# Kernel tuning notes

Measured on AMD Instinct MI355X. Metric: run time of the kernel, lower is better.

## Reference

```python
import jax, jax.numpy as jnp
import numpy as np

N_NODES = 100000
N_EDGES = 3200000
IN_FEATS = 128
OUT_FEATS = 64


def setup_inputs() -> dict:
    key = jax.random.key(0)
    k1, k2, k3, k4 = jax.random.split(key, 4)
    in_feat = jax.random.normal(k1, (N_NODES, IN_FEATS), dtype=jnp.float32)
    src = jax.random.randint(k2, (N_EDGES,), 0, N_NODES, dtype=jnp.int64)
    dst = jax.random.randint(k3, (N_EDGES,), 0, N_NODES, dtype=jnp.int64)
    W = jax.random.normal(k4, (IN_FEATS, OUT_FEATS), dtype=jnp.float32) / np.sqrt(IN_FEATS)
    b = jnp.zeros((OUT_FEATS,), dtype=jnp.float32)
    return {"in_feat": in_feat, "src": src, "dst": dst, "W": W, "b": b}


def reference(in_feat, src, dst, W, b):
    n = in_feat.shape[0]
    ones = jnp.ones_like(src, dtype=in_feat.dtype)
    # DGL GraphConv norm='both': scale by out-degree(src)^-1/2 before agg,
    # in-degree(dst)^-1/2 after agg. Clamp degree to >=1 for isolated nodes.
    deg_out = jnp.maximum(jax.ops.segment_sum(ones, src, num_segments=n), 1.0)
    deg_in = jnp.maximum(jax.ops.segment_sum(ones, dst, num_segments=n), 1.0)
    # in_feats > out_feats => apply W first (mult-first path in DGL)
    xw = in_feat @ W  # [N, out]
    msg = xw[src] * jax.lax.rsqrt(deg_out)[src][:, None]  # [E, out]
    agg = jax.ops.segment_sum(msg, dst, num_segments=n)  # [N, out]
    h = agg * jax.lax.rsqrt(deg_in)[:, None] + b
    return jax.nn.relu(h)
```

## Files before the change

### kernel.cpp

```cpp
#include <hip/hip_runtime.h>
#include <hip/hip_bf16.h>


constexpr int N_NODES = 100000;
constexpr int N_EDGES = 3200000;
constexpr int IN_F    = 128;
constexpr int OUT_F   = 64;
constexpr int BUCKET_NODES = 256;
constexpr int NB   = (N_NODES + BUCKET_NODES - 1) / BUCKET_NODES;
constexpr int CAPB = 10240;
constexpr int C_CHUNK  = 4096;
constexpr int C_BLOCKS = (N_EDGES + C_CHUNK - 1) / C_CHUNK;
constexpr int R_TILE   = 16;

__global__ __launch_bounds__(512) void partition_kernel(
        const int* __restrict__ src, const int* __restrict__ dst,
        int* __restrict__ bucket_cnt, int* __restrict__ bucket_cnt2,
        unsigned* __restrict__ pairs, unsigned char* __restrict__ sbytes) {
    __shared__ int l_cnt [NB], l_base [NB], l_pos [NB], g_base [NB];
    __shared__ int l_cnt2[NB], l_base2[NB], l_pos2[NB], g_base2[NB];
    __shared__ int wsum_s[8];
    __shared__ unsigned buf[C_CHUNK];
    __shared__ unsigned short bkt_of[C_CHUNK];
    __shared__ unsigned char  bbuf[C_CHUNK];
    __shared__ unsigned short bkt2_of[C_CHUNK];
    const int tid  = threadIdx.x;
    const int lane = tid & 63;
    const int wid  = tid >> 6;
    const long e0 = (long)blockIdx.x * C_CHUNK;
    const int  cn = (int)min((long)C_CHUNK, (long)N_EDGES - e0);

    for (int i = tid; i < NB; i += 512) { l_cnt[i] = 0; l_cnt2[i] = 0; }
    __syncthreads();

    unsigned r_pk[8];
    short    r_bk[8];
    #pragma unroll
    for (int k = 0; k < 8; ++k) {
        int i = tid + k * 512;
        r_bk[k] = -1;
        if (i < cn) {
            int d = dst[e0 + i];
            int s = src[e0 + i];
            int bk = d >> 8;
            r_bk[k] = (short)bk;
            r_pk[k] = ((unsigned)(d & 255) << 17) | (unsigned)s;
            atomicAdd(&l_cnt[bk], 1);
            atomicAdd(&l_cnt2[s >> 8], 1);
        }
    }
    __syncthreads();

    {
        int v = (tid < NB) ? l_cnt[tid] : 0;
        int inc = v;
        #pragma unroll
        for (int off = 1; off < 64; off <<= 1) {
            int t = __shfl_up(inc, off);
            if (lane >= off) inc += t;
        }
        if (lane == 63) wsum_s[wid] = inc;
        __syncthreads();
        int woff = 0;
        #pragma unroll
        for (int w = 0; w < 8; ++w) if (w < wid) woff += wsum_s[w];
        int excl = woff + inc - v;
        if (tid < NB) {
            l_base[tid] = excl;
            l_pos[tid]  = excl;
            g_base[tid] = v ? atomicAdd(&bucket_cnt[tid], v) : 0;
        }
    }
    __syncthreads();
    {
        int v = (tid < NB) ? l_cnt2[tid] : 0;
        int inc = v;
        #pragma unroll
        for (int off = 1; off < 64; off <<= 1) {
            int t = __shfl_up(inc, off);
            if (lane >= off) inc += t;
        }
        if (lane == 63) wsum_s[wid] = inc;
        __syncthreads();
        int woff = 0;
        #pragma unroll
        for (int w = 0; w < 8; ++w) if (w < wid) woff += wsum_s[w];
        int excl = woff + inc - v;
        if (tid < NB) {
            l_base2[tid] = excl;
            l_pos2[tid]  = excl;
            g_base2[tid] = v ? atomicAdd(&bucket_cnt2[tid], v) : 0;
        }
    }
    __syncthreads();

    #pragma unroll
    for (int k = 0; k < 8; ++k) {
        if (r_bk[k] >= 0) {
            unsigned pk = r_pk[k];
            int p = atomicAdd(&l_pos[(int)r_bk[k]], 1);
            buf[p] = pk;
            bkt_of[p] = (unsigned short)r_bk[k];
            int bk2 = (int)((pk >> 8) & 0x1FF);
            int p2 = atomicAdd(&l_pos2[bk2], 1);
            bbuf[p2] = (unsigned char)(pk & 255);
            bkt2_of[p2] = (unsigned short)bk2;
        }
    }
    __syncthreads();

    for (int i = tid; i < cn; i += 512) {
        int bk = bkt_of[i];
        int gp = g_base[bk] + (i - l_base[bk]);
        if (gp < CAPB)
            pairs[(long)bk * CAPB + gp] = buf[i];
        int b2 = bkt2_of[i];
        int gp2 = g_base2[b2] + (i - l_base2[b2]);
        if (gp2 < CAPB)
            sbytes[(long)b2 * CAPB + gp2] = bbuf[i];
    }
}

__global__ __launch_bounds__(256) void count_kernel(
        const unsigned char* __restrict__ sbytes, const int* __restrict__ bucket_cnt2,
        int* __restrict__ deg_out_i) {
    __shared__ int hist[BUCKET_NODES];
    const int tid = threadIdx.x;
    const int bk  = blockIdx.x;
    hist[tid] = 0;
    __syncthreads();

    const int cnt = min(bucket_cnt2[bk], CAPB);
    const unsigned* sb4 = (const unsigned*)(sbytes + (long)bk * CAPB);
    const int n4 = cnt >> 2;
    for (int i = tid; i < n4; i += 256) {
        unsigned u = sb4[i];
        atomicAdd(&hist[u & 255], 1);
        atomicAdd(&hist[(u >> 8) & 255], 1);
        atomicAdd(&hist[(u >> 16) & 255], 1);
        atomicAdd(&hist[u >> 24], 1);
    }
    for (int i = (n4 << 2) + tid; i < cnt; i += 256)
        atomicAdd(&hist[sbytes[(long)bk * CAPB + i]], 1);
    __syncthreads();

    const int node = bk * BUCKET_NODES + tid;
    if (node < N_NODES) deg_out_i[node] = hist[tid];
}

__global__ __launch_bounds__(256) void gemm_scale_kernel(
        const float* __restrict__ x, const float* __restrict__ W,
        const int* __restrict__ deg_out_i, __hip_bfloat16* __restrict__ sxw) {
    __shared__ float Wl[IN_F * OUT_F];
    __shared__ float xl[R_TILE * IN_F];
    const int tid = threadIdx.x;
    for (int i = tid; i < IN_F * OUT_F; i += 256) Wl[i] = W[i];

    const int sub = tid >> 6;
    const int col = tid & 63;
    const int n_groups = N_NODES / R_TILE;

    for (int g = blockIdx.x; g < n_groups; g += gridDim.x) {
        __syncthreads();
        const float4* xg = (const float4*)(x + (long)g * R_TILE * IN_F);
        float4* xl4 = (float4*)xl;
        xl4[tid]       = xg[tid];
        xl4[tid + 256] = xg[tid + 256];
        __syncthreads();

        float a0 = 0.0f, a1 = 0.0f, a2 = 0.0f, a3 = 0.0f;
        const float* xr = &xl[sub * 4 * IN_F];
        #pragma unroll
        for (int k4 = 0; k4 < IN_F / 4; ++k4) {
            float4 x0 = ((const float4*)xr)[k4];
            float4 x1 = ((const float4*)(xr + IN_F))[k4];
            float4 x2 = ((const float4*)(xr + 2 * IN_F))[k4];
            float4 x3 = ((const float4*)(xr + 3 * IN_F))[k4];
            float w0 = Wl[(k4 * 4 + 0) * OUT_F + col];
            float w1 = Wl[(k4 * 4 + 1) * OUT_F + col];
            float w2 = Wl[(k4 * 4 + 2) * OUT_F + col];
            float w3 = Wl[(k4 * 4 + 3) * OUT_F + col];
            a0 += x0.x * w0 + x0.y * w1 + x0.z * w2 + x0.w * w3;
            a1 += x1.x * w0 + x1.y * w1 + x1.z * w2 + x1.w * w3;
            a2 += x2.x * w0 + x2.y * w1 + x2.z * w2 + x2.w * w3;
            a3 += x3.x * w0 + x3.y * w1 + x3.z * w2 + x3.w * w3;
        }

        const int r0 = g * R_TILE + sub * 4;
        int d0 = deg_out_i[r0 + 0], d1 = deg_out_i[r0 + 1];
        int d2 = deg_out_i[r0 + 2], d3 = deg_out_i[r0 + 3];
        float s0 = rsqrtf((float)(d0 < 1 ? 1 : d0));
        float s1 = rsqrtf((float)(d1 < 1 ? 1 : d1));
        float s2 = rsqrtf((float)(d2 < 1 ? 1 : d2));
        float s3 = rsqrtf((float)(d3 < 1 ? 1 : d3));
        sxw[(long)(r0 + 0) * OUT_F + col] = __float2bfloat16(a0 * s0);
        sxw[(long)(r0 + 1) * OUT_F + col] = __float2bfloat16(a1 * s1);
        sxw[(long)(r0 + 2) * OUT_F + col] = __float2bfloat16(a2 * s2);
        sxw[(long)(r0 + 3) * OUT_F + col] = __float2bfloat16(a3 * s3);
    }
}

__global__ __launch_bounds__(512) void csr_kernel(
        unsigned* __restrict__ pairs, const int* __restrict__ bucket_cnt,
        int* __restrict__ row_beg, int* __restrict__ row_deg) {
    __shared__ int hist[BUCKET_NODES];
    __shared__ int cur[BUCKET_NODES];
    __shared__ int wsum[4];
    __shared__ unsigned buf[CAPB];
    const int tid  = threadIdx.x;
    const int lane = tid & 63;
    const int wid  = tid >> 6;
    const int bk   = blockIdx.x;
    const long base = (long)bk * CAPB;
    const int cnt  = min(bucket_cnt[bk], CAPB);

    if (tid < 256) hist[tid] = 0;
    __syncthreads();

    for (int i = tid; i < cnt; i += 512) {
        unsigned e = pairs[base + i];
        buf[i] = e;
        atomicAdd(&hist[e >> 17], 1);
    }
    __syncthreads();

    int v = (tid < 256) ? hist[tid] : 0;
    int inc = v;
    #pragma unroll
    for (int off = 1; off < 64; off <<= 1) {
        int t = __shfl_up(inc, off);
        if (lane >= off) inc += t;
    }
    if (tid < 256 && lane == 63) wsum[wid] = inc;
    __syncthreads();
    if (tid < 256) {
        int woff = 0;
        #pragma unroll
        for (int w = 0; w < 4; ++w) if (w < wid) woff += wsum[w];
        int excl = woff + inc - v;
        cur[tid] = excl;
        const int node = bk * BUCKET_NODES + tid;
        if (node < N_NODES) {
            row_beg[node] = (int)(base + excl);
            row_deg[node] = v;
        }
    }
    __syncthreads();

    for (int i = tid; i < cnt; i += 512) {
        unsigned e = buf[i];
        int p = atomicAdd(&cur[e >> 17], 1);
        pairs[base + p] = e & 0x1FFFF;
    }
}

#define ACC8(u)                                   \
    a0 += __uint_as_float((u).x << 16);           \
    a1 += __uint_as_float((u).x & 0xFFFF0000u);   \
    a2 += __uint_as_float((u).y << 16);           \
    a3 += __uint_as_float((u).y & 0xFFFF0000u);   \
    a4 += __uint_as_float((u).z << 16);           \
    a5 += __uint_as_float((u).z & 0xFFFF0000u);   \
    a6 += __uint_as_float((u).w << 16);           \
    a7 += __uint_as_float((u).w & 0xFFFF0000u);

__global__ __launch_bounds__(256) void gather_kernel(
        const int* __restrict__ row_beg, const int* __restrict__ row_deg,
        const unsigned* __restrict__ csr_src, const uint4* __restrict__ sxw4,
        const float* __restrict__ b, float* __restrict__ out) {
    const int lane = threadIdx.x & 63;
    const int node = blockIdx.x * 4 + (threadIdx.x >> 6);
    if (node >= N_NODES) return;

    const int eo = lane >> 3;
    const int c  = lane & 7;

    const int beg = row_beg[node];
    const int deg = row_deg[node];
    const int end = beg + deg;

    float a0 = 0, a1 = 0, a2 = 0, a3 = 0, a4 = 0, a5 = 0, a6 = 0, a7 = 0;

    int j = beg;
    for (; j + 16 <= end; j += 16) {
        unsigned sA = csr_src[j + eo];
        unsigned sB = csr_src[j + 8 + eo];
        uint4 uA = sxw4[(long)sA * 8 + c];
        uint4 uB = sxw4[(long)sB * 8 + c];
        ACC8(uA)
        ACC8(uB)
    }
    for (; j + 8 <= end; j += 8) {
        unsigned s = csr_src[j + eo];
        uint4 u = sxw4[(long)s * 8 + c];
        ACC8(u)
    }
    if (j < end) {
        int e = j + eo;
        if (e < end) {
            unsigned s = csr_src[e];
            uint4 u = sxw4[(long)s * 8 + c];
            ACC8(u)
        }
    }

    #pragma unroll
    for (int off = 8; off < 64; off <<= 1) {
        a0 += __shfl_xor(a0, off);
        a1 += __shfl_xor(a1, off);
        a2 += __shfl_xor(a2, off);
        a3 += __shfl_xor(a3, off);
        a4 += __shfl_xor(a4, off);
        a5 += __shfl_xor(a5, off);
        a6 += __shfl_xor(a6, off);
        a7 += __shfl_xor(a7, off);
    }

    if (lane < 8) {
        float d = (float)(deg < 1 ? 1 : deg);
        float s = rsqrtf(d);
        float4 b0 = ((const float4*)b)[c * 2];
        float4 b1 = ((const float4*)b)[c * 2 + 1];
        float4 o0, o1;
        o0.x = a0 * s + b0.x; o0.x = o0.x > 0.0f ? o0.x : 0.0f;
        o0.y = a1 * s + b0.y; o0.y = o0.y > 0.0f ? o0.y : 0.0f;
        o0.z = a2 * s + b0.z; o0.z = o0.z > 0.0f ? o0.z : 0.0f;
        o0.w = a3 * s + b0.w; o0.w = o0.w > 0.0f ? o0.w : 0.0f;
        o1.x = a4 * s + b1.x; o1.x = o1.x > 0.0f ? o1.x : 0.0f;
        o1.y = a5 * s + b1.y; o1.y = o1.y > 0.0f ? o1.y : 0.0f;
        o1.z = a6 * s + b1.z; o1.z = o1.z > 0.0f ? o1.z : 0.0f;
        o1.w = a7 * s + b1.w; o1.w = o1.w > 0.0f ? o1.w : 0.0f;
        float4* orow = (float4*)(out + (long)node * OUT_F);
        orow[c * 2]     = o0;
        orow[c * 2 + 1] = o1;
    }
}

extern "C" void kernel_launch(void* const* d_in, const int* in_sizes, int n_in,
                              void* d_out, int out_size, void* d_ws, size_t ws_size,
                              hipStream_t stream) {
    const float* in_feat = (const float*)d_in[0];
    const int*   src     = (const int*)d_in[1];
    const int*   dst     = (const int*)d_in[2];
    const float* W       = (const float*)d_in[3];
    const float* b       = (const float*)d_in[4];
    float*       out     = (float*)d_out;

    __hip_bfloat16* sxw         = (__hip_bfloat16*)d_ws;
    int*            deg_out_i   = (int*)(sxw + (size_t)N_NODES * OUT_F);
    int*            bucket_cnt  = deg_out_i + N_NODES;
    int*            bucket_cnt2 = bucket_cnt + NB;
    int*            row_beg     = bucket_cnt2 + NB;
    int*            row_deg     = row_beg + N_NODES;
    unsigned*       pairs       = (unsigned*)(row_deg + N_NODES);
    unsigned char*  sbytes      = (unsigned char*)(pairs + (size_t)NB * CAPB);

    hipMemsetAsync(bucket_cnt, 0, 2 * (size_t)NB * sizeof(int), stream);

    partition_kernel<<<C_BLOCKS, 512, 0, stream>>>(src, dst, bucket_cnt,
                                                   bucket_cnt2, pairs, sbytes);

    count_kernel<<<NB, 256, 0, stream>>>(sbytes, bucket_cnt2, deg_out_i);

    gemm_scale_kernel<<<2048, 256, 0, stream>>>(in_feat, W, deg_out_i, sxw);

    csr_kernel<<<NB, 512, 0, stream>>>(pairs, bucket_cnt, row_beg, row_deg);

    gather_kernel<<<(N_NODES + 3) / 4, 256, 0, stream>>>(row_beg, row_deg, pairs,
                                                         (const uint4*)sxw, b, out);
}
```

Baseline: 269.2 us.

## Merge CSR build and GEMM into one launch, vectorize loads, widen gather unroll

The CSR-building kernel and the scaled GEMM kernel become one launch: the first NB blocks build CSR rows and the rest compute the bf16 transform with 32-row tiles. This removes a launch and lets the two independent stages run side by side. The partition and CSR loads become int4/uint4 vector loads, and the gather unroll goes from 16 to 32 edges per iteration for more memory-level parallelism. The gather's bounds check is dropped, which relies on N_NODES being divisible by 4. The GEMM blocks now share a 512-thread, 48KB-LDS shape, which may change occupancy.

```diff
diff --git a/kernel.cpp b/kernel.cpp
--- a/kernel.cpp
+++ b/kernel.cpp
@@ -11,7 +11,9 @@
 constexpr int CAPB = 10240;
 constexpr int C_CHUNK  = 4096;
 constexpr int C_BLOCKS = (N_EDGES + C_CHUNK - 1) / C_CHUNK;
-constexpr int R_TILE   = 16;
+constexpr int G_TILE   = 32;
+constexpr int G_BLOCKS = 1024;
+constexpr int G_GROUPS = N_NODES / G_TILE;
 
 __global__ __launch_bounds__(512) void partition_kernel(
         const int* __restrict__ src, const int* __restrict__ dst,
@@ -29,24 +31,35 @@
     const int wid  = tid >> 6;
     const long e0 = (long)blockIdx.x * C_CHUNK;
     const int  cn = (int)min((long)C_CHUNK, (long)N_EDGES - e0);
+    const int  cn4 = cn >> 2;
 
     for (int i = tid; i < NB; i += 512) { l_cnt[i] = 0; l_cnt2[i] = 0; }
     __syncthreads();
 
     unsigned r_pk[8];
     short    r_bk[8];
+    const int4* d4p = (const int4*)(dst + e0);
+    const int4* s4p = (const int4*)(src + e0);
     #pragma unroll
-    for (int k = 0; k < 8; ++k) {
-        int i = tid + k * 512;
-        r_bk[k] = -1;
-        if (i < cn) {
-            int d = dst[e0 + i];
-            int s = src[e0 + i];
-            int bk = d >> 8;
-            r_bk[k] = (short)bk;
-            r_pk[k] = ((unsigned)(d & 255) << 17) | (unsigned)s;
-            atomicAdd(&l_cnt[bk], 1);
-            atomicAdd(&l_cnt2[s >> 8], 1);
+    for (int k = 0; k < 2; ++k) {
+        int i4 = tid + k * 512;
+        int rb = k * 4;
+        if (i4 < cn4) {
+            int4 d4 = d4p[i4];
+            int4 s4 = s4p[i4];
+            int dd[4] = {d4.x, d4.y, d4.z, d4.w};
+            int ss[4] = {s4.x, s4.y, s4.z, s4.w};
+            #pragma unroll
+            for (int j = 0; j < 4; ++j) {
+                int bk = dd[j] >> 8;
+                r_bk[rb + j] = (short)bk;
+                r_pk[rb + j] = ((unsigned)(dd[j] & 255) << 17) | (unsigned)ss[j];
+                atomicAdd(&l_cnt[bk], 1);
+                atomicAdd(&l_cnt2[ss[j] >> 8], 1);
+            }
+        } else {
+            #pragma unroll
+            for (int j = 0; j < 4; ++j) r_bk[rb + j] = -1;
         }
     }
     __syncthreads();
@@ -148,109 +161,120 @@
     if (node < N_NODES) deg_out_i[node] = hist[tid];
 }
 
-__global__ __launch_bounds__(256) void gemm_scale_kernel(
+__global__ __launch_bounds__(512) void mega_kernel(
+        unsigned* __restrict__ pairs, const int* __restrict__ bucket_cnt,
+        int* __restrict__ row_beg, int* __restrict__ row_deg,
         const float* __restrict__ x, const float* __restrict__ W,
         const int* __restrict__ deg_out_i, __hip_bfloat16* __restrict__ sxw) {
-    __shared__ float Wl[IN_F * OUT_F];
-    __shared__ float xl[R_TILE * IN_F];
+    alignas(16) __shared__ char smem[49152];
     const int tid = threadIdx.x;
-    for (int i = tid; i < IN_F * OUT_F; i += 256) Wl[i] = W[i];
-
-    const int sub = tid >> 6;
-    const int col = tid & 63;
-    const int n_groups = N_NODES / R_TILE;
-
-    for (int g = blockIdx.x; g < n_groups; g += gridDim.x) {
-        __syncthreads();
-        const float4* xg = (const float4*)(x + (long)g * R_TILE * IN_F);
-        float4* xl4 = (float4*)xl;
-        xl4[tid]       = xg[tid];
-        xl4[tid + 256] = xg[tid + 256];
-        __syncthreads();
-
-        float a0 = 0.0f, a1 = 0.0f, a2 = 0.0f, a3 = 0.0f;
-        const float* xr = &xl[sub * 4 * IN_F];
-        #pragma unroll
-        for (int k4 = 0; k4 < IN_F / 4; ++k4) {
-            float4 x0 = ((const float4*)xr)[k4];
-            float4 x1 = ((const float4*)(xr + IN_F))[k4];
-            float4 x2 = ((const float4*)(xr + 2 * IN_F))[k4];
-            float4 x3 = ((const float4*)(xr + 3 * IN_F))[k4];
-            float w0 = Wl[(k4 * 4 + 0) * OUT_F + col];
-            float w1 = Wl[(k4 * 4 + 1) * OUT_F + col];
-            float w2 = Wl[(k4 * 4 + 2) * OUT_F + col];
-            float w3 = Wl[(k4 * 4 + 3) * OUT_F + col];
-            a0 += x0.x * w0 + x0.y * w1 + x0.z * w2 + x0.w * w3;
-            a1 += x1.x * w0 + x1.y * w1 + x1.z * w2 + x1.w * w3;
-            a2 += x2.x * w0 + x2.y * w1 + x2.z * w2 + x2.w * w3;
-            a3 += x3.x * w0 + x3.y * w1 + x3.z * w2 + x3.w * w3;
-        }
-
-        const int r0 = g * R_TILE + sub * 4;
-        int d0 = deg_out_i[r0 + 0], d1 = deg_out_i[r0 + 1];
-        int d2 = deg_out_i[r0 + 2], d3 = deg_out_i[r0 + 3];
-        float s0 = rsqrtf((float)(d0 < 1 ? 1 : d0));
-        float s1 = rsqrtf((float)(d1 < 1 ? 1 : d1));
-        float s2 = rsqrtf((float)(d2 < 1 ? 1 : d2));
-        float s3 = rsqrtf((float)(d3 < 1 ? 1 : d3));
-        sxw[(long)(r0 + 0) * OUT_F + col] = __float2bfloat16(a0 * s0);
-        sxw[(long)(r0 + 1) * OUT_F + col] = __float2bfloat16(a1 * s1);
-        sxw[(long)(r0 + 2) * OUT_F + col] = __float2bfloat16(a2 * s2);
-        sxw[(long)(r0 + 3) * OUT_F + col] = __float2bfloat16(a3 * s3);
-    }
-}
-
-__global__ __launch_bounds__(512) void csr_kernel(
-        unsigned* __restrict__ pairs, const int* __restrict__ bucket_cnt,
-        int* __restrict__ row_beg, int* __restrict__ row_deg) {
-    __shared__ int hist[BUCKET_NODES];
-    __shared__ int cur[BUCKET_NODES];
-    __shared__ int wsum[4];
-    __shared__ unsigned buf[CAPB];
-    const int tid  = threadIdx.x;
-    const int lane = tid & 63;
-    const int wid  = tid >> 6;
-    const int bk   = blockIdx.x;
-    const long base = (long)bk * CAPB;
-    const int cnt  = min(bucket_cnt[bk], CAPB);
-
-    if (tid < 256) hist[tid] = 0;
-    __syncthreads();
-
-    for (int i = tid; i < cnt; i += 512) {
-        unsigned e = pairs[base + i];
-        buf[i] = e;
-        atomicAdd(&hist[e >> 17], 1);
-    }
-    __syncthreads();
-
-    int v = (tid < 256) ? hist[tid] : 0;
-    int inc = v;
-    #pragma unroll
-    for (int off = 1; off < 64; off <<= 1) {
-        int t = __shfl_up(inc, off);
-        if (lane >= off) inc += t;
-    }
-    if (tid < 256 && lane == 63) wsum[wid] = inc;
-    __syncthreads();
-    if (tid < 256) {
-        int woff = 0;
-        #pragma unroll
-        for (int w = 0; w < 4; ++w) if (w < wid) woff += wsum[w];
-        int excl = woff + inc - v;
-        cur[tid] = excl;
-        const int node = bk * BUCKET_NODES + tid;
-        if (node < N_NODES) {
-            row_beg[node] = (int)(base + excl);
-            row_deg[node] = v;
-        }
-    }
-    __syncthreads();
-
-    for (int i = tid; i < cnt; i += 512) {
-        unsigned e = buf[i];
-        int p = atomicAdd(&cur[e >> 17], 1);
-        pairs[base + p] = e & 0x1FFFF;
+
+    if (blockIdx.x < NB) {
+        unsigned* buf  = (unsigned*)smem;
+        int*      hist = (int*)(smem + 40960);
+        int*      cur  = (int*)(smem + 40960 + 1024);
+        int*      wsum = (int*)(smem + 40960 + 2048);
+        const int lane = tid & 63;
+        const int wid  = tid >> 6;
+        const int bk   = blockIdx.x;
+        const long base = (long)bk * CAPB;
+        const int cnt  = min(bucket_cnt[bk], CAPB);
+
+        if (tid < 256) hist[tid] = 0;
+        __syncthreads();
+
+        const int c4 = cnt >> 2;
+        const uint4* p4 = (const uint4*)(pairs + base);
+        for (int i4 = tid; i4 < c4; i4 += 512) {
+            uint4 e4 = p4[i4];
+            ((uint4*)buf)[i4] = e4;
+            atomicAdd(&hist[e4.x >> 17], 1);
+            atomicAdd(&hist[e4.y >> 17], 1);
+            atomicAdd(&hist[e4.z >> 17], 1);
+            atomicAdd(&hist[e4.w >> 17], 1);
+        }
+        for (int i = (c4 << 2) + tid; i < cnt; i += 512) {
+            unsigned e = pairs[base + i];
+            buf[i] = e;
+            atomicAdd(&hist[e >> 17], 1);
+        }
+        __syncthreads();
+
+        int v = (tid < 256) ? hist[tid] : 0;
+        int inc = v;
+        #pragma unroll
+        for (int off = 1; off < 64; off <<= 1) {
+            int t = __shfl_up(inc, off);
+            if (lane >= off) inc += t;
+        }
+        if (tid < 256 && lane == 63) wsum[wid] = inc;
+        __syncthreads();
+        if (tid < 256) {
+            int woff = 0;
+            #pragma unroll
+            for (int w = 0; w < 4; ++w) if (w < wid) woff += wsum[w];
+            int excl = woff + inc - v;
+            cur[tid] = excl;
+            const int node = bk * BUCKET_NODES + tid;
+            if (node < N_NODES) {
+                row_beg[node] = (int)(base + excl);
+                row_deg[node] = v;
+            }
+        }
+        __syncthreads();
+
+        for (int i = tid; i < cnt; i += 512) {
+            unsigned e = buf[i];
+            int p = atomicAdd(&cur[e >> 17], 1);
+            pairs[base + p] = e & 0x1FFFF;
+        }
+    } else {
+        float* Wl = (float*)smem;
+        float* xl = (float*)(smem + 32768);
+        for (int i = tid; i < IN_F * OUT_F; i += 512) Wl[i] = W[i];
+
+        const int sub = tid >> 6;
+        const int col = tid & 63;
+        const int bid = blockIdx.x - NB;
+
+        for (int g = bid; g < G_GROUPS; g += G_BLOCKS) {
+            __syncthreads();
+            const float4* xg = (const float4*)(x + (long)g * G_TILE * IN_F);
+            float4* xl4 = (float4*)xl;
+            xl4[tid]       = xg[tid];
+            xl4[tid + 512] = xg[tid + 512];
+            __syncthreads();
+
+            float a0 = 0.0f, a1 = 0.0f, a2 = 0.0f, a3 = 0.0f;
+            const float* xr = xl + sub * 4 * IN_F;
+            #pragma unroll
+            for (int k4 = 0; k4 < IN_F / 4; ++k4) {
+                float4 x0 = ((const float4*)xr)[k4];
+                float4 x1 = ((const float4*)(xr + IN_F))[k4];
+                float4 x2 = ((const float4*)(xr + 2 * IN_F))[k4];
+                float4 x3 = ((const float4*)(xr + 3 * IN_F))[k4];
+                float w0 = Wl[(k4 * 4 + 0) * OUT_F + col];
+                float w1 = Wl[(k4 * 4 + 1) * OUT_F + col];
+                float w2 = Wl[(k4 * 4 + 2) * OUT_F + col];
+                float w3 = Wl[(k4 * 4 + 3) * OUT_F + col];
+                a0 += x0.x * w0 + x0.y * w1 + x0.z * w2 + x0.w * w3;
+                a1 += x1.x * w0 + x1.y * w1 + x1.z * w2 + x1.w * w3;
+                a2 += x2.x * w0 + x2.y * w1 + x2.z * w2 + x2.w * w3;
+                a3 += x3.x * w0 + x3.y * w1 + x3.z * w2 + x3.w * w3;
+            }
+
+            const int r0 = g * G_TILE + sub * 4;
+            int d0 = deg_out_i[r0 + 0], d1 = deg_out_i[r0 + 1];
+            int d2 = deg_out_i[r0 + 2], d3 = deg_out_i[r0 + 3];
+            float s0 = rsqrtf((float)(d0 < 1 ? 1 : d0));
+            float s1 = rsqrtf((float)(d1 < 1 ? 1 : d1));
+            float s2 = rsqrtf((float)(d2 < 1 ? 1 : d2));
+            float s3 = rsqrtf((float)(d3 < 1 ? 1 : d3));
+            sxw[(long)(r0 + 0) * OUT_F + col] = __float2bfloat16(a0 * s0);
+            sxw[(long)(r0 + 1) * OUT_F + col] = __float2bfloat16(a1 * s1);
+            sxw[(long)(r0 + 2) * OUT_F + col] = __float2bfloat16(a2 * s2);
+            sxw[(long)(r0 + 3) * OUT_F + col] = __float2bfloat16(a3 * s3);
+        }
     }
 }
 
@@ -270,7 +294,6 @@
         const float* __restrict__ b, float* __restrict__ out) {
     const int lane = threadIdx.x & 63;
     const int node = blockIdx.x * 4 + (threadIdx.x >> 6);
-    if (node >= N_NODES) return;
 
     const int eo = lane >> 3;
     const int c  = lane & 7;
@@ -282,13 +305,16 @@
     float a0 = 0, a1 = 0, a2 = 0, a3 = 0, a4 = 0, a5 = 0, a6 = 0, a7 = 0;
 
     int j = beg;
-    for (; j + 16 <= end; j += 16) {
-        unsigned sA = csr_src[j + eo];
-        unsigned sB = csr_src[j + 8 + eo];
-        uint4 uA = sxw4[(long)sA * 8 + c];
-        uint4 uB = sxw4[(long)sB * 8 + c];
-        ACC8(uA)
-        ACC8(uB)
+    for (; j + 32 <= end; j += 32) {
+        unsigned s0 = csr_src[j + eo];
+        unsigned s1 = csr_src[j + 8 + eo];
+        unsigned s2 = csr_src[j + 16 + eo];
+        unsigned s3 = csr_src[j + 24 + eo];
+        uint4 u0 = sxw4[(long)s0 * 8 + c];
+        uint4 u1 = sxw4[(long)s1 * 8 + c];
+        uint4 u2 = sxw4[(long)s2 * 8 + c];
+        uint4 u3 = sxw4[(long)s3 * 8 + c];
+        ACC8(u0) ACC8(u1) ACC8(u2) ACC8(u3)
     }
     for (; j + 8 <= end; j += 8) {
         unsigned s = csr_src[j + eo];
@@ -362,10 +388,10 @@
 
     count_kernel<<<NB, 256, 0, stream>>>(sbytes, bucket_cnt2, deg_out_i);
 
-    gemm_scale_kernel<<<2048, 256, 0, stream>>>(in_feat, W, deg_out_i, sxw);
-
-    csr_kernel<<<NB, 512, 0, stream>>>(pairs, bucket_cnt, row_beg, row_deg);
-
-    gather_kernel<<<(N_NODES + 3) / 4, 256, 0, stream>>>(row_beg, row_deg, pairs,
-                                                         (const uint4*)sxw, b, out);
-}
+    mega_kernel<<<NB + G_BLOCKS, 512, 0, stream>>>(pairs, bucket_cnt,
+                                                   row_beg, row_deg,
+                                                   in_feat, W, deg_out_i, sxw);
+
+    gather_kernel<<<N_NODES / 4, 256, 0, stream>>>(row_beg, row_deg, pairs,
+                                                   (const uint4*)sxw, b, out);
+}
```

New measurement: 259.3 us. 3.7% less time.
